# Performance work log

Measured on AMD Instinct MI355X. Metric: run time of the kernel, lower is better.

## Reference

```python
import jax, jax.numpy as jnp
import numpy as np

N, D, C = 16384, 64, 128
MARGIN = 1.0
EPS_NORM = 1e-6   # F.normalize eps
EPS_PD = 1e-6     # F.pairwise_distance eps (added to the difference elementwise)


def setup_inputs() -> dict:
    key = jax.random.key(0)
    embeddings = jax.random.normal(key, (N, D), dtype=jnp.float32)
    labels = (jnp.arange(N) % C).astype(jnp.int32).reshape(N, 1)
    # deterministic valid positive: same label (i % C), different index
    pos_idx = ((jnp.arange(N) + C) % N).astype(jnp.int32)
    return {"embeddings": embeddings, "labels": labels, "pos_idx": pos_idx}


def reference(embeddings, labels, pos_idx):
    # L2-normalize rows (torch F.normalize: x / max(||x||, eps))
    nrm = jnp.linalg.norm(embeddings, axis=1, keepdims=True)
    e = embeddings / jnp.maximum(nrm, EPS_NORM)

    lab = labels[:, 0]
    # torch pairwise_distance computes ||x1 - x2 + eps||_2, eps added per element:
    # ||xi - xj + eps||^2 = ||xi||^2 + ||xj||^2 - 2 xi.xj + 2*eps*(sum(xi)-sum(xj)) + D*eps^2
    sq = jnp.sum(e * e, axis=1)          # [N]
    s = jnp.sum(e, axis=1)               # [N]
    gram = e @ e.T                        # [N, N]
    d2 = (sq[:, None] + sq[None, :] - 2.0 * gram
          + 2.0 * EPS_PD * (s[:, None] - s[None, :]) + D * EPS_PD * EPS_PD)
    d2 = jnp.maximum(d2, 0.0)
    dist = jnp.sqrt(jnp.maximum(d2, 1e-12))  # guard sqrt grad at 0

    # one positive per anchor: squared distance
    pos_loss = jnp.sum(d2[jnp.arange(N), pos_idx])

    # all negatives per anchor: hinge^2 on (margin - dist)
    neg_mask = lab[:, None] != lab[None, :]
    hinge = jnp.maximum(MARGIN - dist, 0.0)
    neg_loss = jnp.sum(jnp.where(neg_mask, hinge * hinge, 0.0))

    n_comparisons = N + jnp.sum(neg_mask)
    return (pos_loss + neg_loss) / n_comparisons.astype(jnp.float32)
```

## Files before the change

### kernel.cpp

```cpp
#include <hip/hip_runtime.h>
#include <hip/hip_bf16.h>

#define NN 16384
#define DD 64
#define NBI 32
#define NUNITS 2112
#define NBLK 512
#define NPOSB (NN/4)
#define SCREEN_T 0.49f

constexpr float F_EPS_PD   = 1e-6f;
constexpr float F_EPS_NORM = 1e-6f;

using bf16x8 = __attribute__((ext_vector_type(8))) short;
using f32x4  = __attribute__((ext_vector_type(4))) float;
typedef __attribute__((address_space(1))) const unsigned int gu32_t;
typedef __attribute__((address_space(3))) unsigned int       lu32_t;

__device__ __forceinline__ float wave_sum_f(float v) {
    #pragma unroll
    for (int o = 32; o >= 1; o >>= 1) v += __shfl_xor(v, o);
    return v;
}

__device__ __forceinline__ int band_off(int I) { return 2 * I * (65 - I); }

__global__ __launch_bounds__(256) void norm_kernel(
    const float* __restrict__ emb, const int* __restrict__ pidx,
    const int* __restrict__ lab, float2* __restrict__ up,
    float2* __restrict__ vcp, __hip_bfloat16* __restrict__ ebf,
    float* __restrict__ posP) {
    int w    = threadIdx.x >> 6;
    int row  = blockIdx.x * 4 + w;
    int lane = threadIdx.x & 63;
    int j    = pidx[row];
    float x  = emb[(size_t)row * DD + lane];
    float xj = emb[(size_t)j   * DD + lane];

    float n2  = wave_sum_f(x * x);
    float sx  = wave_sum_f(x);
    float n2j = wave_sum_f(xj * xj);
    float sxj = wave_sum_f(xj);
    float dot = wave_sum_f(x * xj);

    float m  = fmaxf(sqrtf(n2),  F_EPS_NORM);
    float mj = fmaxf(sqrtf(n2j), F_EPS_NORM);
    ebf[(size_t)row * DD + lane] = __float2bfloat16(x / m);

    __shared__ float spos[4];
    if (lane == 0) {
        float sq  = n2 / (m * m);
        float sqj = n2j / (mj * mj);
        float s   = sx / m;
        float sj  = sxj / mj;
        float g   = dot / (m * mj);
        float lf  = (float)lab[row];
        up[row]  = make_float2(sq + 2.0f * F_EPS_PD * s, lf);
        vcp[row] = make_float2(
            sq - 2.0f * F_EPS_PD * s + (float)DD * F_EPS_PD * F_EPS_PD, lf);
        float d2p = sq + sqj - 2.0f * g + 2.0f * F_EPS_PD * (s - sj)
                  + (float)DD * F_EPS_PD * F_EPS_PD;
        spos[w] = fmaxf(d2p, 0.0f);
    }
    __syncthreads();
    if (threadIdx.x == 0)
        posP[blockIdx.x] = spos[0] + spos[1] + spos[2] + spos[3];
}

__device__ __forceinline__ void stage_tile(const short* ebf, const float2* vcp,
                                           int tile, short* slotB, float2* slotV,
                                           int w, int lane) {
    const short* tbase = ebf + (size_t)tile * (128 * DD);
    int rlo = lane >> 3;
    int g   = (lane & 7) ^ rlo;
    #pragma unroll
    for (int q = 0; q < 2; ++q) {
        int m = w * 2 + q;
        __builtin_amdgcn_global_load_lds(
            (gu32_t*)(const void*)(tbase + (size_t)(8 * m + rlo) * DD + g * 8),
            (lu32_t*)(void*)(slotB + m * 512), 16, 0, 0);
    }
    __builtin_amdgcn_global_load_lds(
        (gu32_t*)(const void*)(vcp + (size_t)tile * 128 + lane * 2),
        (lu32_t*)(void*)slotV, 16, 0, 0);
}

#define LOADQ(B, t0_)                                                          \
    do {                                                                       \
        const short* r0_ = lb + ((t0_) * 16 + lrow) * 64;                      \
        const short* r1_ = lb + (((t0_) + 1) * 16 + lrow) * 64;                \
        B[0][0] = *(const bf16x8*)(r0_ + c0s);                                 \
        B[0][1] = *(const bf16x8*)(r0_ + c1s);                                 \
        B[1][0] = *(const bf16x8*)(r1_ + c0s);                                 \
        B[1][1] = *(const bf16x8*)(r1_ + c1s);                                 \
    } while (0)

#define COMPQ(B, t0_)                                                          \
    do {                                                                       \
        _Pragma("unroll")                                                      \
        for (int tt_ = 0; tt_ < 2; ++tt_) {                                    \
            __builtin_amdgcn_s_setprio(1);                                     \
            f32x4 c4[4];                                                       \
            _Pragma("unroll")                                                  \
            for (int s_ = 0; s_ < 4; ++s_) {                                   \
                f32x4 z_ = {0.f, 0.f, 0.f, 0.f};                               \
                z_ = __builtin_amdgcn_mfma_f32_16x16x32_bf16(a[s_][0], B[tt_][0], z_, 0, 0, 0); \
                z_ = __builtin_amdgcn_mfma_f32_16x16x32_bf16(a[s_][1], B[tt_][1], z_, 0, 0, 0); \
                c4[s_] = z_;                                                   \
            }                                                                  \
            __builtin_amdgcn_s_setprio(0);                                     \
            float m0_ = fmaxf(fmaxf(c4[0][0], c4[0][1]), fmaxf(c4[0][2], c4[0][3])); \
            float m1_ = fmaxf(fmaxf(c4[1][0], c4[1][1]), fmaxf(c4[1][2], c4[1][3])); \
            float m2_ = fmaxf(fmaxf(c4[2][0], c4[2][1]), fmaxf(c4[2][2], c4[2][3])); \
            float m3_ = fmaxf(fmaxf(c4[3][0], c4[3][1]), fmaxf(c4[3][2], c4[3][3])); \
            float mx_ = fmaxf(fmaxf(m0_, m1_), fmaxf(m2_, m3_));               \
            if (__any(mx_ > SCREEN_T)) {              \
                float2 vl_ = lv[((t0_) + tt_) * 16 + lrow];                    \
                _Pragma("unroll")                                              \
                for (int s_ = 0; s_ < 4; ++s_) {                               \
                    _Pragma("unroll")                                          \
                    for (int r_ = 0; r_ < 4; ++r_) {                           \
                        float2 ul_ = uband[w * 64 + 16 * s_ + lkh * 4 + r_];   \
                        float d2_ = fmaf(-2.0f, c4[s_][r_], ul_.x + vl_.x);    \
                        float d_  = sqrtf(fmaxf(d2_, 1e-12f));                 \
                        float h_  = fmaxf(1.0f - d_, 0.0f);                    \
                        if (ul_.y != vl_.y) hp = fmaf(h_, h_, hp);             \
                    }                                                          \
                }                                                              \
            }                                                                  \
        }                                                                      \
    } while (0)

__global__ __launch_bounds__(512, 2) void pair_kernel(
    const short* __restrict__ ebf, const float2* __restrict__ up,
    const float2* __restrict__ vcp, float* __restrict__ negP) {
    __shared__ short  ringB[3][8192];
    __shared__ float2 ringV[3][128];
    __shared__ float2 uband[512];
    __shared__ float  sred[8];
    int tid  = threadIdx.x;
    int w    = tid >> 6;
    int lane = tid & 63;
    int lrow = lane & 15, lkh = lane >> 4;
    int c0s  = ((lkh)     ^ (lrow & 7)) * 8;
    int c1s  = ((lkh + 4) ^ (lrow & 7)) * 8;

    int ks = (int)(((long long)blockIdx.x * NUNITS) / NBLK);
    int ke = (int)(((long long)(blockIdx.x + 1) * NUNITS) / NBLK);

    int I = (int)((65.0f - sqrtf(4225.0f - 2.0f * (float)ks)) * 0.5f);
    I = I < 0 ? 0 : (I > NBI - 1 ? NBI - 1 : I);
    while (band_off(I) > ks) --I;
    while (I < NBI - 1 && band_off(I + 1) <= ks) ++I;

    float hacc = 0.0f;
    int u0 = ks;
    while (u0 < ke) {
        int bend = band_off(I + 1);
        int n    = (ke < bend ? ke : bend) - u0;
        int tj0  = 4 * I + (u0 - band_off(I));
        int rowbase = I * 512 + w * 64;
        int rt      = 4 * I + (w >> 1);

        bf16x8 a[4][2];
        #pragma unroll
        for (int s = 0; s < 4; ++s) {
            const short* ab = ebf + (size_t)(rowbase + 16 * s + lrow) * DD + lkh * 8;
            a[s][0] = *(const bf16x8*)(ab);
            a[s][1] = *(const bf16x8*)(ab + 32);
        }
        if (w < 4)
            __builtin_amdgcn_global_load_lds(
                (gu32_t*)(const void*)(up + (size_t)I * 512 + w * 128 + lane * 2),
                (lu32_t*)(void*)(uband + w * 128), 16, 0, 0);
        stage_tile(ebf, vcp, tj0, &ringB[0][0], &ringV[0][0], w, lane);
        if (n > 1)
            stage_tile(ebf, vcp, tj0 + 1, &ringB[1][0], &ringV[1][0], w, lane);

        int sl = 0;
        for (int k = 0; k < n; ++k) {
            if (k + 1 < n) asm volatile("s_waitcnt vmcnt(3)" ::: "memory");
            else           asm volatile("s_waitcnt vmcnt(0)" ::: "memory");
            __builtin_amdgcn_s_barrier();
            __builtin_amdgcn_sched_barrier(0);
            int sl2 = (sl >= 1) ? sl - 1 : 2;
            if (k + 2 < n)
                stage_tile(ebf, vcp, tj0 + k + 2, &ringB[sl2][0], &ringV[sl2][0],
                           w, lane);

            int tj = tj0 + k;
            float wgt = (tj == rt) ? 1.0f : ((tj > rt) ? 2.0f : 0.0f);
            if (wgt != 0.0f) {
                const short*  lb = &ringB[sl][0];
                const float2* lv = &ringV[sl][0];
                float hp = 0.0f;
                bf16x8 Q0[2][2], Q1[2][2];
                LOADQ(Q0, 0);
                LOADQ(Q1, 2);
                COMPQ(Q0, 0);
                LOADQ(Q0, 4);
                COMPQ(Q1, 2);
                LOADQ(Q1, 6);
                COMPQ(Q0, 4);
                COMPQ(Q1, 6);
                hacc = fmaf(wgt, hp, hacc);
            }
            sl = (sl + 1 == 3) ? 0 : sl + 1;
        }
        __builtin_amdgcn_s_barrier();
        __builtin_amdgcn_sched_barrier(0);
        u0 += n;
        ++I;
    }

    hacc = wave_sum_f(hacc);
    if (lane == 0) sred[w] = hacc;
    __syncthreads();
    if (tid == 0) {
        float tn = 0.f;
        #pragma unroll
        for (int i = 0; i < 8; ++i) tn += sred[i];
        negP[blockIdx.x] = tn;
    }
}

__global__ __launch_bounds__(1024) void reduce_kernel(
    const float* __restrict__ posP, const float* __restrict__ negP,
    const int* __restrict__ lab, float* __restrict__ out) {
    __shared__ unsigned int hist[4][1024];
    int t = threadIdx.x;
    int w = t >> 6, lane = t & 63;
    for (int i = t; i < 4096; i += 1024) hist[i >> 10][i & 1023] = 0u;
    __syncthreads();
    const int4* lab4 = (const int4*)lab;
    for (int i = t; i < NN / 4; i += 1024) {
        int4 v = lab4[i];
        atomicAdd(&hist[w & 3][v.x & 1023], 1u);
        atomicAdd(&hist[w & 3][v.y & 1023], 1u);
        atomicAdd(&hist[w & 3][v.z & 1023], 1u);
        atomicAdd(&hist[w & 3][v.w & 1023], 1u);
    }
    __syncthreads();

    float ps = 0.f, ns = 0.f;
    unsigned long long sqc = 0u;
    const float4* posP4 = (const float4*)posP;
    for (int i = t; i < NPOSB / 4; i += 1024) {
        float4 v = posP4[i];
        ps += (v.x + v.y) + (v.z + v.w);
    }
    if (t < NBLK) ns = negP[t];
    {
        unsigned long long h = (unsigned long long)hist[0][t & 1023] + hist[1][t & 1023]
                             + hist[2][t & 1023] + hist[3][t & 1023];
        sqc = h * h;
    }

    ps = wave_sum_f(ps);
    ns = wave_sum_f(ns);
    #pragma unroll
    for (int o = 32; o >= 1; o >>= 1) sqc += __shfl_xor(sqc, o);

    __shared__ float sp[16], sn[16];
    __shared__ unsigned long long sc[16];
    if (lane == 0) { sp[w] = ps; sn[w] = ns; sc[w] = sqc; }
    __syncthreads();
    if (t == 0) {
        float pos = 0.f, neg = 0.f;
        unsigned long long s2 = 0;
        #pragma unroll
        for (int i = 0; i < 16; ++i) { pos += sp[i]; neg += sn[i]; s2 += sc[i]; }
        unsigned long long nneg = (unsigned long long)NN * NN - s2;
        float ncomp = (float)((unsigned long long)NN + nneg);
        out[0] = (pos + neg) / ncomp;
    }
}

extern "C" void kernel_launch(void* const* d_in, const int* in_sizes, int n_in,
                              void* d_out, int out_size, void* d_ws, size_t ws_size,
                              hipStream_t stream) {
    const float* emb = (const float*)d_in[0];
    const int* lab   = (const int*)d_in[1];
    const int* pidx  = (const int*)d_in[2];
    float* out = (float*)d_out;
    char* ws = (char*)d_ws;
    float2*         up   = (float2*)(ws);
    float2*         vcp  = (float2*)(ws + 131072);
    __hip_bfloat16* ebf  = (__hip_bfloat16*)(ws + 262144);
    float*          posP = (float*)(ws + 2359296);
    float*          negP = (float*)(ws + 2375680);

    norm_kernel<<<NPOSB, 256, 0, stream>>>(emb, pidx, lab, up, vcp, ebf, posP);
    pair_kernel<<<NBLK, 512, 0, stream>>>((const short*)ebf, up, vcp, negP);
    reduce_kernel<<<1, 1024, 0, stream>>>(posP, negP, lab, out);
}
```

Measured before the change: 52.77 us.

## Fuse final reduction into pair kernel via last-block atomic completion

Removes the separate single-block reduce kernel. The label histogram and positive-loss sum are now built with global atomics inside the norm kernel, which processes 32 rows per 512-thread block. The pair kernel adds its partial sums atomically, and the last block to finish, detected with a done counter, computes the final loss. This saves a kernel launch and the serial tail of the reduce pass, at the cost of a memset, global atomic contention and nondeterministic float summation order.

```diff
diff --git a/kernel.cpp b/kernel.cpp
--- a/kernel.cpp
+++ b/kernel.cpp
@@ -6,7 +6,6 @@
 #define NBI 32
 #define NUNITS 2112
 #define NBLK 512
-#define NPOSB (NN/4)
 #define SCREEN_T 0.49f
 
 constexpr float F_EPS_PD   = 1e-6f;
@@ -25,46 +24,55 @@
 
 __device__ __forceinline__ int band_off(int I) { return 2 * I * (65 - I); }
 
-__global__ __launch_bounds__(256) void norm_kernel(
+__global__ __launch_bounds__(512) void norm_kernel(
     const float* __restrict__ emb, const int* __restrict__ pidx,
     const int* __restrict__ lab, float2* __restrict__ up,
     float2* __restrict__ vcp, __hip_bfloat16* __restrict__ ebf,
-    float* __restrict__ posP) {
-    int w    = threadIdx.x >> 6;
-    int row  = blockIdx.x * 4 + w;
-    int lane = threadIdx.x & 63;
-    int j    = pidx[row];
-    float x  = emb[(size_t)row * DD + lane];
-    float xj = emb[(size_t)j   * DD + lane];
-
-    float n2  = wave_sum_f(x * x);
-    float sx  = wave_sum_f(x);
-    float n2j = wave_sum_f(xj * xj);
-    float sxj = wave_sum_f(xj);
-    float dot = wave_sum_f(x * xj);
-
-    float m  = fmaxf(sqrtf(n2),  F_EPS_NORM);
-    float mj = fmaxf(sqrtf(n2j), F_EPS_NORM);
-    ebf[(size_t)row * DD + lane] = __float2bfloat16(x / m);
-
-    __shared__ float spos[4];
-    if (lane == 0) {
-        float sq  = n2 / (m * m);
-        float sqj = n2j / (mj * mj);
-        float s   = sx / m;
-        float sj  = sxj / mj;
-        float g   = dot / (m * mj);
-        float lf  = (float)lab[row];
-        up[row]  = make_float2(sq + 2.0f * F_EPS_PD * s, lf);
-        vcp[row] = make_float2(
-            sq - 2.0f * F_EPS_PD * s + (float)DD * F_EPS_PD * F_EPS_PD, lf);
-        float d2p = sq + sqj - 2.0f * g + 2.0f * F_EPS_PD * (s - sj)
-                  + (float)DD * F_EPS_PD * F_EPS_PD;
-        spos[w] = fmaxf(d2p, 0.0f);
-    }
+    unsigned int* __restrict__ hist, float* __restrict__ posTotal) {
+    int tid  = threadIdx.x;
+    int w    = tid >> 6;
+    int lane = tid & 63;
+    float pospart = 0.f;
+    int rbase = blockIdx.x * 32 + w * 4;
+    for (int r = 0; r < 4; ++r) {
+        int row = rbase + r;
+        int j   = pidx[row];
+        float x  = emb[(size_t)row * DD + lane];
+        float xj = emb[(size_t)j   * DD + lane];
+        float n2  = wave_sum_f(x * x);
+        float sx  = wave_sum_f(x);
+        float n2j = wave_sum_f(xj * xj);
+        float sxj = wave_sum_f(xj);
+        float dot = wave_sum_f(x * xj);
+        float m = fmaxf(sqrtf(n2), F_EPS_NORM);
+        ebf[(size_t)row * DD + lane] = __float2bfloat16(x / m);
+        if (lane == 0) {
+            float mj  = fmaxf(sqrtf(n2j), F_EPS_NORM);
+            float sq  = n2 / (m * m);
+            float sqj = n2j / (mj * mj);
+            float s   = sx / m;
+            float sj  = sxj / mj;
+            float g   = dot / (m * mj);
+            int   li  = lab[row];
+            float lf  = (float)li;
+            up[row]  = make_float2(sq + 2.0f * F_EPS_PD * s, lf);
+            vcp[row] = make_float2(
+                sq - 2.0f * F_EPS_PD * s + (float)DD * F_EPS_PD * F_EPS_PD, lf);
+            float d2p = sq + sqj - 2.0f * g + 2.0f * F_EPS_PD * (s - sj)
+                      + (float)DD * F_EPS_PD * F_EPS_PD;
+            pospart += fmaxf(d2p, 0.0f);
+            atomicAdd(&hist[li & 1023], 1u);
+        }
+    }
+    __shared__ float sred[8];
+    if (lane == 0) sred[w] = pospart;
     __syncthreads();
-    if (threadIdx.x == 0)
-        posP[blockIdx.x] = spos[0] + spos[1] + spos[2] + spos[3];
+    if (tid == 0) {
+        float t = 0.f;
+        #pragma unroll
+        for (int i = 0; i < 8; ++i) t += sred[i];
+        atomicAdd(posTotal, t);
+    }
 }
 
 __device__ __forceinline__ void stage_tile(const short* ebf, const float2* vcp,
@@ -133,11 +141,14 @@
 
 __global__ __launch_bounds__(512, 2) void pair_kernel(
     const short* __restrict__ ebf, const float2* __restrict__ up,
-    const float2* __restrict__ vcp, float* __restrict__ negP) {
+    const float2* __restrict__ vcp, const unsigned int* __restrict__ hist,
+    float* __restrict__ posTotal, float* __restrict__ negTotal,
+    unsigned int* done, float* __restrict__ out) {
     __shared__ short  ringB[3][8192];
     __shared__ float2 ringV[3][128];
     __shared__ float2 uband[512];
     __shared__ float  sred[8];
+    __shared__ unsigned int isLast;
     int tid  = threadIdx.x;
     int w    = tid >> 6;
     int lane = tid & 63;
@@ -220,59 +231,37 @@
         float tn = 0.f;
         #pragma unroll
         for (int i = 0; i < 8; ++i) tn += sred[i];
-        negP[blockIdx.x] = tn;
-    }
-}
-
-__global__ __launch_bounds__(1024) void reduce_kernel(
-    const float* __restrict__ posP, const float* __restrict__ negP,
-    const int* __restrict__ lab, float* __restrict__ out) {
-    __shared__ unsigned int hist[4][1024];
-    int t = threadIdx.x;
-    int w = t >> 6, lane = t & 63;
-    for (int i = t; i < 4096; i += 1024) hist[i >> 10][i & 1023] = 0u;
+        atomicAdd(negTotal, tn);
+        __threadfence();
+        unsigned int prev = __hip_atomic_fetch_add(done, 1u, __ATOMIC_ACQ_REL,
+                                                   __HIP_MEMORY_SCOPE_AGENT);
+        isLast = (prev == NBLK - 1) ? 1u : 0u;
+    }
     __syncthreads();
-    const int4* lab4 = (const int4*)lab;
-    for (int i = t; i < NN / 4; i += 1024) {
-        int4 v = lab4[i];
-        atomicAdd(&hist[w & 3][v.x & 1023], 1u);
-        atomicAdd(&hist[w & 3][v.y & 1023], 1u);
-        atomicAdd(&hist[w & 3][v.z & 1023], 1u);
-        atomicAdd(&hist[w & 3][v.w & 1023], 1u);
-    }
-    __syncthreads();
-
-    float ps = 0.f, ns = 0.f;
-    unsigned long long sqc = 0u;
-    const float4* posP4 = (const float4*)posP;
-    for (int i = t; i < NPOSB / 4; i += 1024) {
-        float4 v = posP4[i];
-        ps += (v.x + v.y) + (v.z + v.w);
-    }
-    if (t < NBLK) ns = negP[t];
-    {
-        unsigned long long h = (unsigned long long)hist[0][t & 1023] + hist[1][t & 1023]
-                             + hist[2][t & 1023] + hist[3][t & 1023];
-        sqc = h * h;
-    }
-
-    ps = wave_sum_f(ps);
-    ns = wave_sum_f(ns);
-    #pragma unroll
-    for (int o = 32; o >= 1; o >>= 1) sqc += __shfl_xor(sqc, o);
-
-    __shared__ float sp[16], sn[16];
-    __shared__ unsigned long long sc[16];
-    if (lane == 0) { sp[w] = ps; sn[w] = ns; sc[w] = sqc; }
-    __syncthreads();
-    if (t == 0) {
-        float pos = 0.f, neg = 0.f;
-        unsigned long long s2 = 0;
-        #pragma unroll
-        for (int i = 0; i < 16; ++i) { pos += sp[i]; neg += sn[i]; s2 += sc[i]; }
-        unsigned long long nneg = (unsigned long long)NN * NN - s2;
-        float ncomp = (float)((unsigned long long)NN + nneg);
-        out[0] = (pos + neg) / ncomp;
+
+    if (isLast) {
+        unsigned long long sqc = 0;
+        for (int i = tid; i < 1024; i += 512) {
+            unsigned long long h = hist[i];
+            sqc += h * h;
+        }
+        #pragma unroll
+        for (int o = 32; o >= 1; o >>= 1) sqc += __shfl_xor(sqc, o);
+        unsigned long long* sc = (unsigned long long*)&ringV[0][0];
+        if (lane == 0) sc[w] = sqc;
+        __syncthreads();
+        if (tid == 0) {
+            unsigned long long s2 = 0;
+            #pragma unroll
+            for (int i = 0; i < 8; ++i) s2 += sc[i];
+            float pos = __hip_atomic_load(posTotal, __ATOMIC_ACQUIRE,
+                                          __HIP_MEMORY_SCOPE_AGENT);
+            float neg = __hip_atomic_load(negTotal, __ATOMIC_ACQUIRE,
+                                          __HIP_MEMORY_SCOPE_AGENT);
+            unsigned long long nneg = (unsigned long long)NN * NN - s2;
+            float ncomp = (float)((unsigned long long)NN + nneg);
+            out[0] = (pos + neg) / ncomp;
+        }
     }
 }
 
@@ -287,10 +276,14 @@
     float2*         up   = (float2*)(ws);
     float2*         vcp  = (float2*)(ws + 131072);
     __hip_bfloat16* ebf  = (__hip_bfloat16*)(ws + 262144);
-    float*          posP = (float*)(ws + 2359296);
-    float*          negP = (float*)(ws + 2375680);
-
-    norm_kernel<<<NPOSB, 256, 0, stream>>>(emb, pidx, lab, up, vcp, ebf, posP);
-    pair_kernel<<<NBLK, 512, 0, stream>>>((const short*)ebf, up, vcp, negP);
-    reduce_kernel<<<1, 1024, 0, stream>>>(posP, negP, lab, out);
-}
+    unsigned int*   hist = (unsigned int*)(ws + 2359296);
+    float*          posT = (float*)(ws + 2363392);
+    float*          negT = (float*)(ws + 2363396);
+    unsigned int*   done = (unsigned int*)(ws + 2363400);
+
+    hipMemsetAsync(ws + 2359296, 0, 4108, stream);
+    norm_kernel<<<NN / 32, 512, 0, stream>>>(emb, pidx, lab, up, vcp, ebf,
+                                             hist, posT);
+    pair_kernel<<<NBLK, 512, 0, stream>>>((const short*)ebf, up, vcp, hist,
+                                          posT, negT, done, out);
+}
```

New measurement: 94.01 us. 78.2% more time.
